# Optimization experiments

Hardware: AMD Instinct MI355X
Metric: run time of the kernel (lower is better)

The kernel has to match this reference:

```python
import jax, jax.numpy as jnp
import numpy as np

N_NODES = 100000
N_EDGES = 1600000
IN_F = 128
HID_F = 128
OUT_F = 128

def _glorot(key, shape):
    lim = np.sqrt(6.0 / (shape[0] + shape[1]))
    return jax.random.uniform(key, shape, jnp.float32, -lim, lim)

def setup_inputs() -> dict:
    key = jax.random.key(0)
    ks = jax.random.split(key, 9)
    x = jax.random.normal(ks[0], (N_NODES, IN_F), jnp.float32)
    src = jax.random.randint(ks[1], (N_EDGES,), 0, N_NODES, jnp.int32)
    dst = jax.random.randint(ks[2], (N_EDGES,), 0, N_NODES, jnp.int32)
    return {
        'x': x, 'src': src, 'dst': dst,
        'W_self1': _glorot(ks[3], (IN_F, HID_F)),
        'W_neigh1': _glorot(ks[4], (IN_F, HID_F)),
        'b1': jnp.zeros((HID_F,), jnp.float32),
        'W_self2': _glorot(ks[5], (HID_F, OUT_F)),
        'W_neigh2': _glorot(ks[6], (HID_F, OUT_F)),
        'b2': jnp.zeros((OUT_F,), jnp.float32),
    }

def _sage_mean(h, src, dst, W_self, W_neigh, b, n_nodes):
    # mean-aggregate src features onto dst (DGL SAGEConv 'mean')
    msg_sum = jax.ops.segment_sum(h[src], dst, num_segments=n_nodes)  # [N, d]
    deg = jax.ops.segment_sum(jnp.ones_like(dst, jnp.float32), dst, num_segments=n_nodes)
    h_neigh = msg_sum / jnp.maximum(deg, 1.0)[:, None]
    return h @ W_self + h_neigh @ W_neigh + b

def reference(x, src, dst, W_self1, W_neigh1, b1, W_self2, W_neigh2, b2):
    n = x.shape[0]
    h = _sage_mean(x, src, dst, W_self1, W_neigh1, b1, n)
    h = _sage_mean(h, src, dst, W_self2, W_neigh2, b2, n)
    # edge-wise dot product score between endpoint features (u_dot_v)
    s = jnp.sum(h[src] * h[dst], axis=-1)  # [E]
    smin, smax = jnp.min(s), jnp.max(s)
    return (s - smin) / (smax - smin)
```

## Files before the change

### kernel.cpp

```cpp
#include <hip/hip_runtime.h>
#include <hip/hip_bf16.h>

#define F 128

typedef unsigned int uint;
typedef unsigned short ushort;
typedef __attribute__((ext_vector_type(8))) short short8;
typedef __attribute__((ext_vector_type(4))) float f32x4;

__device__ inline ushort f2bf(float f) {
    uint u = __float_as_uint(f);
    u += 0x7FFF + ((u >> 16) & 1);
    return (ushort)(u >> 16);
}
__device__ inline float2 bf2f(uint u) {
    return make_float2(__uint_as_float(u << 16), __uint_as_float(u & 0xFFFF0000u));
}

__global__ __launch_bounds__(256) void rank_kernel(const int* __restrict__ dst,
                                                   int* __restrict__ cnt,
                                                   ushort* __restrict__ rel, int E) {
    int e = blockIdx.x * 256 + threadIdx.x;
    if (e < E) rel[e] = (ushort)atomicAdd(&cnt[dst[e]], 1);
}

__global__ __launch_bounds__(256) void scan_block(const int* __restrict__ cnt,
                                                  int* __restrict__ off,
                                                  int* __restrict__ bsum, int N) {
    __shared__ int t[256];
    int i = blockIdx.x * 256 + threadIdx.x;
    int v = (i < N) ? cnt[i] : 0;
    t[threadIdx.x] = v;
    __syncthreads();
    for (int o = 1; o < 256; o <<= 1) {
        int x = (threadIdx.x >= o) ? t[threadIdx.x - o] : 0;
        __syncthreads();
        t[threadIdx.x] += x;
        __syncthreads();
    }
    if (i < N) off[i] = t[threadIdx.x] - v;
    if (threadIdx.x == 255) bsum[blockIdx.x] = t[255];
}

__global__ __launch_bounds__(512) void scan_sums(int* __restrict__ bsum, int nb) {
    __shared__ int t[512];
    int v = (threadIdx.x < nb) ? bsum[threadIdx.x] : 0;
    t[threadIdx.x] = v;
    __syncthreads();
    for (int o = 1; o < 512; o <<= 1) {
        int x = (threadIdx.x >= o) ? t[threadIdx.x - o] : 0;
        __syncthreads();
        t[threadIdx.x] += x;
        __syncthreads();
    }
    if (threadIdx.x < nb) bsum[threadIdx.x] = t[threadIdx.x] - v;
}

__global__ __launch_bounds__(256) void scan_add_rdeg(int* __restrict__ off,
                                                     const int* __restrict__ bsum,
                                                     const int* __restrict__ cnt,
                                                     float* __restrict__ rdeg, int N) {
    int i = blockIdx.x * 256 + threadIdx.x;
    if (i >= N) return;
    off[i] += bsum[blockIdx.x];
    rdeg[i] = 1.0f / fmaxf((float)cnt[i], 1.0f);
}

__global__ __launch_bounds__(256) void fill_kernel(const int* __restrict__ src,
                                                   const int* __restrict__ dst,
                                                   const int* __restrict__ off,
                                                   const ushort* __restrict__ rel,
                                                   int* __restrict__ srcS, int E) {
    int e = blockIdx.x * 256 + threadIdx.x;
    if (e >= E) return;
    srcS[off[dst[e]] + (int)rel[e]] = src[e];
}

__global__ __launch_bounds__(256) void prep_kernel(const float* __restrict__ x,
                                                   const float* __restrict__ W0,
                                                   const float* __restrict__ W1,
                                                   const float* __restrict__ W2,
                                                   const float* __restrict__ W3,
                                                   uint* __restrict__ xb,
                                                   ushort* __restrict__ Wt, int NF4, int N) {
    int i = blockIdx.x * 256 + threadIdx.x;
    if (i < NF4) {
        float4 v = ((const float4*)x)[i];
        uint ua = (uint)f2bf(v.x) | ((uint)f2bf(v.y) << 16);
        uint ub = (uint)f2bf(v.z) | ((uint)f2bf(v.w) << 16);
        int r = i >> 5;
        int g = i & 31;
        int c = g >> 2;
        int o = (g & 3) * 2;
        uint* dstp = xb + (size_t)c * (size_t)N * 8 + (size_t)r * 8 + o;
        *(uint2*)dstp = make_uint2(ua, ub);
    } else {
        int idx = i - NF4;
        if (idx >= 4 * 16384) return;
        int mat = idx >> 14;
        int pos = idx & 16383;
        int k = pos >> 7, n = pos & 127;
        const float* W = (mat == 0) ? W0 : (mat == 1) ? W1 : (mat == 2) ? W2 : W3;
        Wt[mat * 16384 + n * 128 + k] = f2bf(W[k * 128 + n]);
    }
}

__global__ __launch_bounds__(256) void agg_gather_cm(const uint* __restrict__ hb,
                                                     const int* __restrict__ off,
                                                     const int* __restrict__ srcS,
                                                     const float* __restrict__ rdeg,
                                                     uint* __restrict__ msgb,
                                                     int N, int E) {
    int chunk = blockIdx.x & 7;
    int ngrp = blockIdx.x >> 3;
    int lane = threadIdx.x & 63;
    int sub = lane >> 3;
    int u = lane & 7;
    int node = ngrp * 32 + (threadIdx.x >> 6) * 8 + sub;
    if (node >= N) return;
    const uint* hc = hb + (size_t)chunk * (size_t)N * 8;
    int p = off[node];
    int pe = (node == N - 1) ? E : off[node + 1];
    float2 acc = make_float2(0.f, 0.f);
    if (p < pe) {
        int deg = pe - p;
        int last = pe - 1;
        for (; p < pe; p += 4) {
            int i1 = min(p + 1, last), i2 = min(p + 2, last), i3 = min(p + 3, last);
            int s0 = srcS[p], s1 = srcS[i1], s2 = srcS[i2], s3 = srcS[i3];
            float2 f0 = bf2f(hc[(size_t)s0 * 8 + u]);
            float2 f1 = bf2f(hc[(size_t)s1 * 8 + u]);
            float2 f2 = bf2f(hc[(size_t)s2 * 8 + u]);
            float2 f3 = bf2f(hc[(size_t)s3 * 8 + u]);
            acc.x += (f0.x + f1.x) + (f2.x + f3.x);
            acc.y += (f0.y + f1.y) + (f2.y + f3.y);
        }
        int d = (4 - (deg & 3)) & 3;
        if (d) {
            float2 fl = bf2f(hc[(size_t)srcS[last] * 8 + u]);
            float fd = (float)d;
            acc.x -= fd * fl.x;
            acc.y -= fd * fl.y;
        }
    }
    float rd = rdeg[node];
    msgb[(size_t)chunk * (size_t)N * 8 + (size_t)node * 8 + u] =
        (uint)f2bf(acc.x * rd) | ((uint)f2bf(acc.y * rd) << 16);
}

template <int OUT_CM>
__global__ __launch_bounds__(256) void sage_mfma_t(const uint* __restrict__ hb,
                                                   const uint* __restrict__ mb,
                                                   const uint* __restrict__ Wt,
                                                   const float* __restrict__ bias,
                                                   ushort* __restrict__ outb, int N) {
    int wave = threadIdx.x >> 6, lane = threadIdx.x & 63;
    int m = lane & 15, q = lane >> 4;
    int r0 = blockIdx.x * 64 + wave * 16;
    int arow = r0 + m;
    if (arow >= N) arow = N - 1;

    f32x4 acc[8];
#pragma unroll
    for (int t = 0; t < 8; t++) acc[t] = (f32x4){0.f, 0.f, 0.f, 0.f};

    size_t N8 = (size_t)N * 8;
#pragma unroll
    for (int sel = 0; sel < 2; sel++) {
        const uint* arowp = (sel ? mb : hb) + (size_t)arow * 8 + (q & 1) * 4;
        const uint* wsel = Wt + sel * 8192;
#pragma unroll
        for (int kk = 0; kk < 4; kk++) {
            short8 a = *(const short8*)(arowp + (size_t)(kk * 2 + (q >> 1)) * N8);
            int ko = kk * 16 + q * 4;
#pragma unroll
            for (int t = 0; t < 8; t++) {
                short8 b = *(const short8*)(wsel + (size_t)(16 * t + m) * 64 + ko);
                acc[t] = __builtin_amdgcn_mfma_f32_16x16x32_bf16(a, b, acc[t], 0, 0, 0);
            }
        }
    }

#pragma unroll
    for (int t = 0; t < 8; t++) {
        float bs = bias[16 * t + m];
#pragma unroll
        for (int r = 0; r < 4; r++) {
            int orow = r0 + q * 4 + r;
            if (orow < N) {
                ushort val = f2bf(acc[t][r] + bs);
                if (OUT_CM)
                    outb[(size_t)t * (size_t)N * 16 + (size_t)orow * 16 + m] = val;
                else
                    outb[(size_t)orow * 128 + 16 * t + m] = val;
            }
        }
    }
}

__global__ __launch_bounds__(256) void edge_score_mfma(const uint* __restrict__ hb,
                                                       const int* __restrict__ off,
                                                       const int* __restrict__ srcS,
                                                       float* __restrict__ sc,
                                                       float2* __restrict__ pmm, int N, int E) {
    int node = blockIdx.x * 4 + (threadIdx.x >> 6);
    int lane = threadIdx.x & 63;
    int m = lane & 15, q = lane >> 4;
    float lmin = INFINITY, lmax = -INFINITY;

    if (node < N) {
        int p = off[node];
        int pe = (node == N - 1) ? E : off[node + 1];
        if (p < pe) {
            const uint* nrow = hb + (size_t)node * 64;
            short8 bfr[4];
#pragma unroll
            for (int kk = 0; kk < 4; kk++)
                bfr[kk] = *(const short8*)(nrow + kk * 16 + q * 4);

            for (; p < pe; p += 16) {
                int idx = p + m;
                if (idx >= pe) idx = pe - 1;
                const uint* arow = hb + (size_t)srcS[idx] * 64;
                f32x4 acc = (f32x4){0.f, 0.f, 0.f, 0.f};
#pragma unroll
                for (int kk = 0; kk < 4; kk++) {
                    short8 a = *(const short8*)(arow + kk * 16 + q * 4);
                    acc = __builtin_amdgcn_mfma_f32_16x16x32_bf16(a, bfr[kk], acc, 0, 0, 0);
                }
                if (m == 0) {
                    if (p + 16 <= pe) {
                        *(float4*)(sc + p + q * 4) = make_float4(acc[0], acc[1], acc[2], acc[3]);
                        float mn = fminf(fminf(acc[0], acc[1]), fminf(acc[2], acc[3]));
                        float mx = fmaxf(fmaxf(acc[0], acc[1]), fmaxf(acc[2], acc[3]));
                        lmin = fminf(lmin, mn);
                        lmax = fmaxf(lmax, mx);
                    } else {
#pragma unroll
                        for (int r = 0; r < 4; r++) {
                            int e = p + q * 4 + r;
                            if (e < pe) {
                                sc[e] = acc[r];
                                lmin = fminf(lmin, acc[r]);
                                lmax = fmaxf(lmax, acc[r]);
                            }
                        }
                    }
                }
            }
        }
    }

#pragma unroll
    for (int o = 1; o <= 32; o <<= 1) {
        lmin = fminf(lmin, __shfl_xor(lmin, o));
        lmax = fmaxf(lmax, __shfl_xor(lmax, o));
    }
    __shared__ float smin[4], smax[4];
    int wv = threadIdx.x >> 6;
    if (lane == 0) { smin[wv] = lmin; smax[wv] = lmax; }
    __syncthreads();
    if (threadIdx.x == 0) {
        float mA = fminf(fminf(smin[0], smin[1]), fminf(smin[2], smin[3]));
        float MA = fmaxf(fmaxf(smax[0], smax[1]), fmaxf(smax[2], smax[3]));
        pmm[blockIdx.x] = make_float2(mA, MA);
    }
}

__global__ __launch_bounds__(1024) void minmax_final(const float2* __restrict__ pmm,
                                                     float* __restrict__ mmf, int nb) {
    float vmin = INFINITY, vmax = -INFINITY;
    for (int i = threadIdx.x; i < nb; i += 1024) {
        float2 v = pmm[i];
        vmin = fminf(vmin, v.x);
        vmax = fmaxf(vmax, v.y);
    }
#pragma unroll
    for (int o = 1; o <= 32; o <<= 1) {
        vmin = fminf(vmin, __shfl_xor(vmin, o));
        vmax = fmaxf(vmax, __shfl_xor(vmax, o));
    }
    __shared__ float smin[16], smax[16];
    int lane = threadIdx.x & 63, wv = threadIdx.x >> 6;
    if (lane == 0) { smin[wv] = vmin; smax[wv] = vmax; }
    __syncthreads();
    if (threadIdx.x == 0) {
        float m = smin[0], M = smax[0];
        for (int w = 1; w < 16; w++) { m = fminf(m, smin[w]); M = fmaxf(M, smax[w]); }
        mmf[0] = m;
        mmf[1] = M;
    }
}

__global__ __launch_bounds__(256) void norm_kernel(const float* __restrict__ sc,
                                                   const int* __restrict__ dst,
                                                   const ushort* __restrict__ rel,
                                                   const int* __restrict__ off,
                                                   float* __restrict__ out,
                                                   const float* __restrict__ mmf, int E) {
    float mn = mmf[0];
    float mx = mmf[1];
    float inv = 1.0f / (mx - mn);
    int i = blockIdx.x * 256 + threadIdx.x;
    if (i < E) {
        int p = off[dst[i]] + (int)rel[i];
        out[i] = (sc[p] - mn) * inv;
    }
}

extern "C" void kernel_launch(void* const* d_in, const int* in_sizes, int n_in,
                              void* d_out, int out_size, void* d_ws, size_t ws_size,
                              hipStream_t stream) {
    const float* x   = (const float*)d_in[0];
    const int*   src = (const int*)d_in[1];
    const int*   dst = (const int*)d_in[2];
    const float* Ws1 = (const float*)d_in[3];
    const float* Wn1 = (const float*)d_in[4];
    const float* b1  = (const float*)d_in[5];
    const float* Ws2 = (const float*)d_in[6];
    const float* Wn2 = (const float*)d_in[7];
    const float* b2  = (const float*)d_in[8];

    int N = in_sizes[0] / F;
    int E = in_sizes[1];
    float* out = (float*)d_out;

    int nbN = (N + 255) / 256;
    int nbE = (E + 255) / 256;
    int nbEdgeBlocks = (N + 3) / 4;
    int NF4 = N * F / 4;

    int* off  = (int*)d_ws;
    int* cnt  = off + N;
    int* srcS = cnt + N;
    ushort* rel = (ushort*)(srcS + E);
    float* sc = (float*)((int*)rel + E / 2);
    int* bsum = (int*)(sc + E);
    float* rdeg = (float*)(bsum + 1024);
    float* mmf = (float*)(rdeg + N);
    float2* pmm = (float2*)(mmf + 4);
    uint* Wtb = (uint*)(pmm + 25600);
    size_t elemOff = 3 * (size_t)N + 2 * (size_t)E + (size_t)E / 2 + 1024 + 4 + 51200 + 32768;
    elemOff = (elemOff + 3) & ~(size_t)3;
    uint* xb   = (uint*)d_ws + elemOff;
    uint* msgb = xb + (size_t)N * 64;
    uint* h1b  = msgb + (size_t)N * 64;
    uint* h2b  = h1b + (size_t)N * 64;

    hipMemsetAsync(cnt, 0, (size_t)N * sizeof(int), stream);

    rank_kernel<<<nbE, 256, 0, stream>>>(dst, cnt, rel, E);
    scan_block<<<nbN, 256, 0, stream>>>(cnt, off, bsum, N);
    scan_sums<<<1, 512, 0, stream>>>(bsum, nbN);
    scan_add_rdeg<<<nbN, 256, 0, stream>>>(off, bsum, cnt, rdeg, N);
    fill_kernel<<<nbE, 256, 0, stream>>>(src, dst, off, rel, srcS, E);

    prep_kernel<<<(NF4 + 4 * 16384 + 255) / 256, 256, 0, stream>>>(
        x, Ws1, Wn1, Ws2, Wn2, xb, (ushort*)Wtb, NF4, N);

    int nbAgg = 8 * ((N + 31) / 32);

    agg_gather_cm<<<nbAgg, 256, 0, stream>>>(xb, off, srcS, rdeg, msgb, N, E);
    sage_mfma_t<1><<<(N + 63) / 64, 256, 0, stream>>>(xb, msgb, Wtb, b1, (ushort*)h1b, N);

    agg_gather_cm<<<nbAgg, 256, 0, stream>>>(h1b, off, srcS, rdeg, msgb, N, E);
    sage_mfma_t<0><<<(N + 63) / 64, 256, 0, stream>>>(h1b, msgb, Wtb + 16384, b2, (ushort*)h2b, N);

    edge_score_mfma<<<nbEdgeBlocks, 256, 0, stream>>>(h2b, off, srcS, sc, pmm, N, E);
    minmax_final<<<1, 1024, 0, stream>>>(pmm, mmf, nbEdgeBlocks);
    norm_kernel<<<(E + 255) / 256, 256, 0, stream>>>(sc, dst, rel, off, out, mmf, E);
}
```

Measured before the change: 641.4 us.

## Vectorize gather loads and split edge scoring into chunked partial dot products

The aggregation kernel now has each lane load 16-byte uint4 vectors, four edge slots per node handled in parallel, and reduces across slots with shuffles, replacing the 4-byte-per-lane gathers. Layer-2 output now stays in the chunk-major layout, and edge scoring no longer uses per-node MFMA. It computes per-chunk partial dot products into an 8xE buffer that reuses the xb region, and a new fold kernel sums them and computes block min/max. This is meant to improve gather coalescing and locality within each chunk. In exchange it adds 8xE float partial writes and reads plus an extra kernel launch.

Result: no change. 634.8 us (-1.0%).

```diff
diff --git a/kernel.cpp b/kernel.cpp
--- a/kernel.cpp
+++ b/kernel.cpp
@@ -15,6 +15,28 @@
 }
 __device__ inline float2 bf2f(uint u) {
     return make_float2(__uint_as_float(u << 16), __uint_as_float(u & 0xFFFF0000u));
+}
+__device__ inline void acc8(float* a, uint4 v) {
+    float2 f;
+    f = bf2f(v.x); a[0] += f.x; a[1] += f.y;
+    f = bf2f(v.y); a[2] += f.x; a[3] += f.y;
+    f = bf2f(v.z); a[4] += f.x; a[5] += f.y;
+    f = bf2f(v.w); a[6] += f.x; a[7] += f.y;
+}
+__device__ inline void unp8(float* a, uint4 v) {
+    float2 f;
+    f = bf2f(v.x); a[0] = f.x; a[1] = f.y;
+    f = bf2f(v.y); a[2] = f.x; a[3] = f.y;
+    f = bf2f(v.z); a[4] = f.x; a[5] = f.y;
+    f = bf2f(v.w); a[6] = f.x; a[7] = f.y;
+}
+__device__ inline float dot8(const float* d, uint4 v) {
+    float2 f; float s = 0.f;
+    f = bf2f(v.x); s += f.x * d[0] + f.y * d[1];
+    f = bf2f(v.y); s += f.x * d[2] + f.y * d[3];
+    f = bf2f(v.z); s += f.x * d[4] + f.y * d[5];
+    f = bf2f(v.w); s += f.x * d[6] + f.y * d[7];
+    return s;
 }
 
 __global__ __launch_bounds__(256) void rank_kernel(const int* __restrict__ dst,
@@ -114,46 +136,61 @@
     int chunk = blockIdx.x & 7;
     int ngrp = blockIdx.x >> 3;
     int lane = threadIdx.x & 63;
-    int sub = lane >> 3;
-    int u = lane & 7;
-    int node = ngrp * 32 + (threadIdx.x >> 6) * 8 + sub;
+    int t = lane & 7;
+    int g = lane >> 3;
+    int slot = t >> 1;
+    int half = t & 1;
+    int node = ngrp * 32 + (threadIdx.x >> 6) * 8 + g;
     if (node >= N) return;
     const uint* hc = hb + (size_t)chunk * (size_t)N * 8;
     int p = off[node];
     int pe = (node == N - 1) ? E : off[node + 1];
-    float2 acc = make_float2(0.f, 0.f);
+    float acc[8];
+#pragma unroll
+    for (int j = 0; j < 8; j++) acc[j] = 0.f;
     if (p < pe) {
         int deg = pe - p;
         int last = pe - 1;
-        for (; p < pe; p += 4) {
-            int i1 = min(p + 1, last), i2 = min(p + 2, last), i3 = min(p + 3, last);
-            int s0 = srcS[p], s1 = srcS[i1], s2 = srcS[i2], s3 = srcS[i3];
-            float2 f0 = bf2f(hc[(size_t)s0 * 8 + u]);
-            float2 f1 = bf2f(hc[(size_t)s1 * 8 + u]);
-            float2 f2 = bf2f(hc[(size_t)s2 * 8 + u]);
-            float2 f3 = bf2f(hc[(size_t)s3 * 8 + u]);
-            acc.x += (f0.x + f1.x) + (f2.x + f3.x);
-            acc.y += (f0.y + f1.y) + (f2.y + f3.y);
+        for (; p < pe; p += 8) {
+            int ia = min(p + slot, last);
+            int ib = min(p + 4 + slot, last);
+            int sa = srcS[ia], sb = srcS[ib];
+            uint4 va = *(const uint4*)(hc + (size_t)sa * 8 + half * 4);
+            uint4 vb = *(const uint4*)(hc + (size_t)sb * 8 + half * 4);
+            acc8(acc, va);
+            acc8(acc, vb);
         }
-        int d = (4 - (deg & 3)) & 3;
-        if (d) {
-            float2 fl = bf2f(hc[(size_t)srcS[last] * 8 + u]);
+        int d = (8 - (deg & 7)) & 7;
+        if (d && slot == 0) {
+            uint4 vl = *(const uint4*)(hc + (size_t)srcS[last] * 8 + half * 4);
+            float tmp[8];
+            unp8(tmp, vl);
             float fd = (float)d;
-            acc.x -= fd * fl.x;
-            acc.y -= fd * fl.y;
+#pragma unroll
+            for (int j = 0; j < 8; j++) acc[j] -= fd * tmp[j];
         }
     }
-    float rd = rdeg[node];
-    msgb[(size_t)chunk * (size_t)N * 8 + (size_t)node * 8 + u] =
-        (uint)f2bf(acc.x * rd) | ((uint)f2bf(acc.y * rd) << 16);
-}
-
-template <int OUT_CM>
-__global__ __launch_bounds__(256) void sage_mfma_t(const uint* __restrict__ hb,
-                                                   const uint* __restrict__ mb,
-                                                   const uint* __restrict__ Wt,
-                                                   const float* __restrict__ bias,
-                                                   ushort* __restrict__ outb, int N) {
+#pragma unroll
+    for (int j = 0; j < 8; j++) {
+        acc[j] += __shfl_xor(acc[j], 2);
+        acc[j] += __shfl_xor(acc[j], 4);
+    }
+    if (slot == 0) {
+        float rd = rdeg[node];
+        uint4 w;
+        w.x = (uint)f2bf(acc[0] * rd) | ((uint)f2bf(acc[1] * rd) << 16);
+        w.y = (uint)f2bf(acc[2] * rd) | ((uint)f2bf(acc[3] * rd) << 16);
+        w.z = (uint)f2bf(acc[4] * rd) | ((uint)f2bf(acc[5] * rd) << 16);
+        w.w = (uint)f2bf(acc[6] * rd) | ((uint)f2bf(acc[7] * rd) << 16);
+        *(uint4*)(msgb + (size_t)chunk * (size_t)N * 8 + (size_t)node * 8 + half * 4) = w;
+    }
+}
+
+__global__ __launch_bounds__(256) void sage_mfma(const uint* __restrict__ hb,
+                                                 const uint* __restrict__ mb,
+                                                 const uint* __restrict__ Wt,
+                                                 const float* __restrict__ bias,
+                                                 ushort* __restrict__ outb, int N) {
     int wave = threadIdx.x >> 6, lane = threadIdx.x & 63;
     int m = lane & 15, q = lane >> 4;
     int r0 = blockIdx.x * 64 + wave * 16;
@@ -187,77 +224,72 @@
 #pragma unroll
         for (int r = 0; r < 4; r++) {
             int orow = r0 + q * 4 + r;
-            if (orow < N) {
-                ushort val = f2bf(acc[t][r] + bs);
-                if (OUT_CM)
-                    outb[(size_t)t * (size_t)N * 16 + (size_t)orow * 16 + m] = val;
-                else
-                    outb[(size_t)orow * 128 + 16 * t + m] = val;
-            }
+            if (orow < N)
+                outb[(size_t)t * (size_t)N * 16 + (size_t)orow * 16 + m] = f2bf(acc[t][r] + bs);
         }
     }
 }
 
-__global__ __launch_bounds__(256) void edge_score_mfma(const uint* __restrict__ hb,
-                                                       const int* __restrict__ off,
-                                                       const int* __restrict__ srcS,
-                                                       float* __restrict__ sc,
-                                                       float2* __restrict__ pmm, int N, int E) {
-    int node = blockIdx.x * 4 + (threadIdx.x >> 6);
+__global__ __launch_bounds__(256) void edge_part(const uint* __restrict__ hb,
+                                                 const int* __restrict__ off,
+                                                 const int* __restrict__ srcS,
+                                                 float* __restrict__ pbuf,
+                                                 int N, int E) {
+    int chunk = blockIdx.x & 7;
+    int ngrp = blockIdx.x >> 3;
     int lane = threadIdx.x & 63;
-    int m = lane & 15, q = lane >> 4;
+    int t = lane & 7;
+    int g = lane >> 3;
+    int slot = t >> 1;
+    int half = t & 1;
+    int node = ngrp * 32 + (threadIdx.x >> 6) * 8 + g;
+    if (node >= N) return;
+    const uint* hc = hb + (size_t)chunk * (size_t)N * 8;
+    float* pb = pbuf + (size_t)chunk * (size_t)E;
+    int p = off[node];
+    int pe = (node == N - 1) ? E : off[node + 1];
+    if (p >= pe) return;
+
+    float dF[8];
+    unp8(dF, *(const uint4*)(hc + (size_t)node * 8 + half * 4));
+
+    int last = pe - 1;
+    for (; p < pe; p += 8) {
+        int ia = min(p + slot, last);
+        int ib = min(p + 4 + slot, last);
+        int sa = srcS[ia], sb = srcS[ib];
+        uint4 va = *(const uint4*)(hc + (size_t)sa * 8 + half * 4);
+        uint4 vb = *(const uint4*)(hc + (size_t)sb * 8 + half * 4);
+        float pa = dot8(dF, va);
+        float pc = dot8(dF, vb);
+        pa += __shfl_xor(pa, 1);
+        pc += __shfl_xor(pc, 1);
+        if (half == 0) {
+            if (p + slot <= last) pb[p + slot] = pa;
+            if (p + 4 + slot <= last) pb[p + 4 + slot] = pc;
+        }
+    }
+}
+
+__global__ __launch_bounds__(256) void fold_minmax(const float* __restrict__ pbuf,
+                                                   float* __restrict__ sc,
+                                                   float2* __restrict__ pmm, int E) {
+    int i = blockIdx.x * 256 + threadIdx.x;
     float lmin = INFINITY, lmax = -INFINITY;
-
-    if (node < N) {
-        int p = off[node];
-        int pe = (node == N - 1) ? E : off[node + 1];
-        if (p < pe) {
-            const uint* nrow = hb + (size_t)node * 64;
-            short8 bfr[4];
-#pragma unroll
-            for (int kk = 0; kk < 4; kk++)
-                bfr[kk] = *(const short8*)(nrow + kk * 16 + q * 4);
-
-            for (; p < pe; p += 16) {
-                int idx = p + m;
-                if (idx >= pe) idx = pe - 1;
-                const uint* arow = hb + (size_t)srcS[idx] * 64;
-                f32x4 acc = (f32x4){0.f, 0.f, 0.f, 0.f};
-#pragma unroll
-                for (int kk = 0; kk < 4; kk++) {
-                    short8 a = *(const short8*)(arow + kk * 16 + q * 4);
-                    acc = __builtin_amdgcn_mfma_f32_16x16x32_bf16(a, bfr[kk], acc, 0, 0, 0);
-                }
-                if (m == 0) {
-                    if (p + 16 <= pe) {
-                        *(float4*)(sc + p + q * 4) = make_float4(acc[0], acc[1], acc[2], acc[3]);
-                        float mn = fminf(fminf(acc[0], acc[1]), fminf(acc[2], acc[3]));
-                        float mx = fmaxf(fmaxf(acc[0], acc[1]), fmaxf(acc[2], acc[3]));
-                        lmin = fminf(lmin, mn);
-                        lmax = fmaxf(lmax, mx);
-                    } else {
-#pragma unroll
-                        for (int r = 0; r < 4; r++) {
-                            int e = p + q * 4 + r;
-                            if (e < pe) {
-                                sc[e] = acc[r];
-                                lmin = fminf(lmin, acc[r]);
-                                lmax = fmaxf(lmax, acc[r]);
-                            }
-                        }
-                    }
-                }
-            }
-        }
-    }
-
+    if (i < E) {
+        float v = 0.f;
+#pragma unroll
+        for (int c = 0; c < 8; c++) v += pbuf[(size_t)c * (size_t)E + i];
+        sc[i] = v;
+        lmin = lmax = v;
+    }
 #pragma unroll
     for (int o = 1; o <= 32; o <<= 1) {
         lmin = fminf(lmin, __shfl_xor(lmin, o));
         lmax = fmaxf(lmax, __shfl_xor(lmax, o));
     }
     __shared__ float smin[4], smax[4];
-    int wv = threadIdx.x >> 6;
+    int lane = threadIdx.x & 63, wv = threadIdx.x >> 6;
     if (lane == 0) { smin[wv] = lmin; smax[wv] = lmax; }
     __syncthreads();
     if (threadIdx.x == 0) {
@@ -327,7 +359,6 @@
 
     int nbN = (N + 255) / 256;
     int nbE = (E + 255) / 256;
-    int nbEdgeBlocks = (N + 3) / 4;
     int NF4 = N * F / 4;
 
     int* off  = (int*)d_ws;
@@ -346,6 +377,7 @@
     uint* msgb = xb + (size_t)N * 64;
     uint* h1b  = msgb + (size_t)N * 64;
     uint* h2b  = h1b + (size_t)N * 64;
+    float* pbuf = (float*)xb;
 
     hipMemsetAsync(cnt, 0, (size_t)N * sizeof(int), stream);
 
@@ -361,12 +393,13 @@
     int nbAgg = 8 * ((N + 31) / 32);
 
     agg_gather_cm<<<nbAgg, 256, 0, stream>>>(xb, off, srcS, rdeg, msgb, N, E);
-    sage_mfma_t<1><<<(N + 63) / 64, 256, 0, stream>>>(xb, msgb, Wtb, b1, (ushort*)h1b, N);
+    sage_mfma<<<(N + 63) / 64, 256, 0, stream>>>(xb, msgb, Wtb, b1, (ushort*)h1b, N);
 
     agg_gather_cm<<<nbAgg, 256, 0, stream>>>(h1b, off, srcS, rdeg, msgb, N, E);
-    sage_mfma_t<0><<<(N + 63) / 64, 256, 0, stream>>>(h1b, msgb, Wtb + 16384, b2, (ushort*)h2b, N);
-
-    edge_score_mfma<<<nbEdgeBlocks, 256, 0, stream>>>(h2b, off, srcS, sc, pmm, N, E);
-    minmax_final<<<1, 1024, 0, stream>>>(pmm, mmf, nbEdgeBlocks);
-    norm_kernel<<<(E + 255) / 256, 256, 0, stream>>>(sc, dst, rel, off, out, mmf, E);
-}
+    sage_mfma<<<(N + 63) / 64, 256, 0, stream>>>(h1b, msgb, Wtb + 16384, b2, (ushort*)h2b, N);
+
+    edge_part<<<nbAgg, 256, 0, stream>>>(h2b, off, srcS, pbuf, N, E);
+    fold_minmax<<<nbE, 256, 0, stream>>>(pbuf, sc, pmm, E);
+    minmax_final<<<1, 1024, 0, stream>>>(pmm, mmf, nbE);
+    norm_kernel<<<nbE, 256, 0, stream>>>(sc, dst, rel, off, out, mmf, E);
+}
```
